# Performance work log

Measured on AMD Instinct MI355X. Metric: run time of the kernel, lower is better.

Reference implementation:

```python
import jax, jax.numpy as jnp
import numpy as np

B, N, T = 32, 256, 256
W, H, EMB = 32, 128, 64          # window_size, tgcn_hidden_dim, gsl_embed_dim
K, ALPHA, NC, E = 3, 1.0, 16, 8192  # gsl_avg_steps, gsl_alpha, num_classes, static edges
GCN_IN = W + H                    # GSL gconv in_channels
THRESH = 1e-8


def setup_inputs():
    ks = jax.random.split(jax.random.key(0), 24)
    rng = np.random.default_rng(0)
    src = rng.integers(0, N, size=E)
    tgt = (src + 1 + rng.integers(0, N - 1, size=E)) % N  # no self-loops (PyG adds them)
    edge_index = jnp.asarray(np.stack([src, tgt]), dtype=jnp.int32)

    def p(k, shape):
        return jax.random.normal(k, shape, jnp.float32) * (shape[0] ** -0.5)

    z = lambda n: jnp.zeros((n,), jnp.float32)
    return {
        "x": jax.random.normal(ks[0], (B, N, T), jnp.float32),
        "static_edge_index": edge_index,
        "static_edge_weight": jax.random.uniform(ks[1], (E,), jnp.float32),
        "Wg": p(ks[2], (GCN_IN, EMB)), "bg": z(EMB),
        "W1": p(ks[3], (EMB, EMB)), "b1": z(EMB),
        "W2": p(ks[4], (EMB, EMB)), "b2": z(EMB),
        "Wz": p(ks[5], (W, H)), "bz": z(H),
        "Wr": p(ks[6], (W, H)), "br": z(H),
        "Wh": p(ks[7], (W, H)), "bh": z(H),
        "Wlz": p(ks[8], (2 * H, H)), "blz": z(H),
        "Wlr": p(ks[9], (2 * H, H)), "blr": z(H),
        "Wlh": p(ks[10], (2 * H, H)), "blh": z(H),
        "Wc": p(ks[11], (H * N, NC)), "bc": z(NC),
    }


def _forward(x, edge_index, edge_weight, Wg, bg, W1, b1, W2, b2,
             Wz, bz, Wr, br, Wh, bh, Wlz, blz, Wlr, blr, Wlh, blh, Wc, bc):
    dt = x.dtype
    eye = jnp.eye(N, dtype=dt)

    # Static graph: dense adjacency + self loops, symmetric GCN normalization.
    A = jnp.zeros((N, N), dt).at[edge_index[0], edge_index[1]].add(edge_weight) + eye
    deg = A.sum(0)  # in-degree at targets (col sums)
    di = jnp.where(deg > 0, jax.lax.rsqrt(deg), 0.0)
    S = di[:, None] * A * di[None, :]  # S[r,c]; out[c] = sum_r S[r,c] x[r]

    # windowing: v[t,b,n,:] = x[b,n,t*W:(t+1)*W]
    v = x.reshape(B, N, T // W, W).transpose(2, 0, 1, 3)  # [nw,B,N,W]

    def gcn_norm_b(Ad):  # Ad [B,N,N], zero diagonal guaranteed
        Ah = Ad + eye
        d = Ah.sum(-2)
        q = jnp.where(d > 0, jax.lax.rsqrt(d), 0.0)
        return q[:, :, None] * Ah * q[:, None, :]

    def step(carry, vt):
        h, hist, cnt = carry  # h [B,N,H], hist [K,B,N,N]
        It = jnp.concatenate([vt, h], -1)                   # [B,N,W+H]
        df = jnp.einsum('rc,brf->bcf', S, It @ Wg) + bg     # static GCNConv
        de1 = jnp.tanh(ALPHA * (df @ W1 + b1))
        de2 = jnp.tanh(ALPHA * (df @ W2 + b2))
        M = jnp.einsum('bne,bme->bnm', de1, de2)            # de1 @ de2^T
        Et = jax.nn.relu(jnp.tanh(ALPHA * (M - M.transpose(0, 2, 1))))
        hist = jnp.concatenate([hist[1:], Et[None]], 0)     # deque(maxlen=K)
        cnt = jnp.minimum(cnt + 1, K)
        Mt = hist.sum(0) / cnt.astype(dt)
        An = gcn_norm_b(jnp.where(Mt > THRESH, Mt, jnp.zeros((), dt)))

        def conv(Wk, bk):  # dynamic GCNConv, block-diag == per-batch dense
            return jnp.einsum('brc,brf->bcf', An, vt @ Wk) + bk

        Z = jax.nn.sigmoid(jnp.concatenate([conv(Wz, bz), h], -1) @ Wlz + blz)
        R = jax.nn.sigmoid(jnp.concatenate([conv(Wr, br), h], -1) @ Wlr + blr)
        Ht = jnp.tanh(jnp.concatenate([conv(Wh, bh), h * R], -1) @ Wlh + blh)
        h = Z * h + (1.0 - Z) * Ht
        return (h, hist, cnt), None

    h0 = jnp.zeros((B, N, H), dt)
    hist0 = jnp.zeros((K, B, N, N), dt)
    (h, _, _), _ = jax.lax.scan(step, (h0, hist0, jnp.int32(0)), v)
    return h.reshape(B, N * H) @ Wc + bc  # [B, NC]


def reference(x, static_edge_index, static_edge_weight, Wg, bg, W1, b1, W2, b2,
              Wz, bz, Wr, br, Wh, bh, Wlz, blz, Wlr, blr, Wlh, blh, Wc, bc):
    return _forward(x, static_edge_index, static_edge_weight, Wg, bg, W1, b1, W2, b2,
                    Wz, bz, Wr, br, Wh, bh, Wlz, blz, Wlr, blr, Wlh, blh, Wc, bc)
```

## Files before the change

kernel.cpp:

```cpp
#include <hip/hip_runtime.h>
#include <hip/hip_bf16.h>
#include <math.h>

#define BB  32
#define NN  256
#define TT  256
#define WW  32
#define HH  128
#define EMBD 64
#define NCLS 16
#define NE  8192

__device__ __forceinline__ float bf(const __hip_bfloat16* p, int i) {
    return __bfloat162float(p[i]);
}
__device__ __forceinline__ float ld3(const void* p, int i, int m) {
    if (m == 2) return (float)((const double*)p)[i];
    if (m == 1) return ((const float*)p)[i];
    return __bfloat162float(((const __hip_bfloat16*)p)[i]);
}
__device__ __forceinline__ float r16(float x) {
    return __bfloat162float(__float2bfloat16(x));
}
__device__ __forceinline__ float tanh_s(float x) {
    x = fminf(20.0f, fmaxf(-20.0f, x));
    return tanhf(x);
}
__device__ __forceinline__ float sig_s(float x) {
    x = fminf(30.0f, fmaxf(-30.0f, x));
    return 1.0f / (1.0f + expf(-x));
}


__global__ __launch_bounds__(64) void k_sentinel(float* out, float v) {
    int i = blockIdx.x * 64 + threadIdx.x;
    if (i < BB * NCLS) out[i] = v;
}

__global__ __launch_bounds__(256) void k_probe_all(
        const void* x, const void* ew, const void* Wg, const void* W1, const void* W2,
        const void* Wz, const void* Wr, const void* Wh, const void* Wlz, const void* Wlr,
        const void* Wlh, const void* Wc, int* insB, int* insF) {
    int sec = blockIdx.x >> 2, sub = blockIdx.x & 3;
    const void* p; int nB, idx;
    switch (sec) {
        case 0:  p = x;   nB = 32768; idx = 0;  break;
        case 1:  p = ew;  nB = 8192;  idx = 2;  break;
        case 2:  p = Wg;  nB = 10240; idx = 3;  break;
        case 3:  p = W1;  nB = 4096;  idx = 5;  break;
        case 4:  p = W2;  nB = 4096;  idx = 7;  break;
        case 5:  p = Wz;  nB = 4096;  idx = 9;  break;
        case 6:  p = Wr;  nB = 4096;  idx = 11; break;
        case 7:  p = Wh;  nB = 4096;  idx = 13; break;
        case 8:  p = Wlz; nB = 32768; idx = 15; break;
        case 9:  p = Wlr; nB = 32768; idx = 17; break;
        case 10: p = Wlh; nB = 32768; idx = 19; break;
        default: p = Wc;  nB = 32768; idx = 21; break;
    }
    int nF = nB >> 2;
    const __hip_bfloat16* pb = (const __hip_bfloat16*)p;
    const float* pf = (const float*)p;
    int start = sub * 256 + threadIdx.x;
    for (int i = start; i < nB; i += 1024) {
        float v = __bfloat162float(pb[i]);
        if (!(fabsf(v) < 64.0f)) { insB[idx] = 1; break; }
    }
    for (int i = start; i < nF; i += 1024) {
        float v = pf[i];
        if (!(fabsf(v) < 1e4f)) { insF[idx] = 1; break; }
    }
}

__global__ void k_resolve(const int* insB, const int* insF, int* modes) {
    int i = threadIdx.x;
    if (i < 32 && i != 1)
        modes[i] = insB[i] ? (insF[i] ? 2 : 1) : 0;
}

__global__ __launch_bounds__(64) void k_detect_ei(const int* ei, int* modes) {
    if (threadIdx.x == 0 && blockIdx.x == 0) {
        bool allz = true;
        for (int k = 1; k < 64; k += 2) if (ei[k] != 0) allz = false;
        modes[1] = allz ? 1 : 0;
    }
}

__global__ __launch_bounds__(256) void k_cvtall(const void* Wg, const void* W1, const void* W2,
                                                const void* Wz, const void* Wr, const void* Wh,
                                                const void* Wlz, const void* Wlr, const void* Wlh,
                                                const void* Wc, const int* modes, float* dst) {
    int i = blockIdx.x * 256 + threadIdx.x;
    if (i >= 665600) return;
    float v;
    if      (i < 10240)  v = ld3(Wg,  i,          modes[3]);
    else if (i < 14336)  v = ld3(W1,  i - 10240,  modes[5]);
    else if (i < 18432)  v = ld3(W2,  i - 14336,  modes[7]);
    else if (i < 22528)  v = ld3(Wz,  i - 18432,  modes[9]);
    else if (i < 26624)  v = ld3(Wr,  i - 22528,  modes[11]);
    else if (i < 30720)  v = ld3(Wh,  i - 26624,  modes[13]);
    else if (i < 63488)  v = ld3(Wlz, i - 30720,  modes[15]);
    else if (i < 96256)  v = ld3(Wlr, i - 63488,  modes[17]);
    else if (i < 129024) v = ld3(Wlh, i - 96256,  modes[19]);
    else if (i < 653312) v = ld3(Wc,  i - 129024, modes[21]);
    else {
        int j = i - 653312, w = j / 384, rem = j - w * 384;
        int g = rem >> 7, f = rem & 127;
        const void* Wk = (g == 0) ? Wz : ((g == 1) ? Wr : Wh);
        int mk = (g == 0) ? modes[9] : ((g == 1) ? modes[11] : modes[13]);
        v = ld3(Wk, w * 128 + f, mk);
    }
    dst[i] = v;
}

__global__ __launch_bounds__(256) void k_fuse(const float* Wzf, const float* Wrf, const float* Whf,
                                              const float* Wlzf, const float* Wlrf, const float* Wlhf,
                                              const __hip_bfloat16* bz, const __hip_bfloat16* br,
                                              const __hip_bfloat16* bh,
                                              const __hip_bfloat16* blz, const __hip_bfloat16* blr,
                                              const __hip_bfloat16* blh,
                                              float* Wf, float* bfv) {
    int g = blockIdx.y;
    const float* Wcv = (g == 0) ? Wzf : ((g == 1) ? Wrf : Whf);
    const float* Wl  = (g == 0) ? Wlzf : ((g == 1) ? Wlrf : Wlhf);
    const __hip_bfloat16* bcv = (g == 0) ? bz : ((g == 1) ? br : bh);
    const __hip_bfloat16* blv = (g == 0) ? blz : ((g == 1) ? blr : blh);
    int idx = blockIdx.x * 256 + threadIdx.x;
    if (idx >= 160 * 128) return;
    int k = idx >> 7, f = idx & 127;
    float v;
    if (k < 32) {
        float acc = 0.f;
        for (int m = 0; m < 128; m++) acc += Wcv[k * 128 + m] * Wl[m * 128 + f];
        v = acc;
    } else {
        v = Wl[(k + 96) * 128 + f];
    }
    Wf[((size_t)g * 160 + k) * 128 + f] = v;
    if (idx < 128) {
        float acc = __bfloat162float(blv[idx]);
        for (int m = 0; m < 128; m++) acc += __bfloat162float(bcv[m]) * Wl[m * 128 + idx];
        bfv[g * 128 + idx] = acc;
    }
}


__global__ __launch_bounds__(256) void k_scatter(const int* ei, const void* ew, float* A,
                                                 const int* modes) {
    int e = blockIdx.x * 256 + threadIdx.x;
    if (e < NE) {
        int s, t;
        if (modes[1]) { s = ei[2 * e]; t = ei[2 * (NE + e)]; }
        else          { s = ei[e];     t = ei[NE + e]; }
        float w = r16(ld3(ew, e, modes[2]));
        if ((unsigned)s < NN && (unsigned)t < NN)
            atomicAdd(&A[s * NN + t], w);
    }
    if (blockIdx.x == 0) atomicAdd(&A[threadIdx.x * NN + threadIdx.x], 1.0f);
}

__global__ __launch_bounds__(256) void k_roundA(float* A) {
    int i = blockIdx.x * 256 + threadIdx.x;
    A[i] = r16(A[i]);
}

__global__ __launch_bounds__(256) void k_di(const float* A, float* di) {
    int wave = threadIdx.x >> 6, lane = threadIdx.x & 63;
    int c = blockIdx.x * 4 + wave;
    float s = 0.f;
    for (int r = lane; r < NN; r += 64) s += A[r * NN + c];
    for (int o = 32; o > 0; o >>= 1) s += __shfl_down(s, o, 64);
    if (lane == 0) {
        float deg = r16(s);
        di[c] = (deg > 0.f) ? r16(1.0f / sqrtf(deg)) : 0.0f;
    }
}

__global__ __launch_bounds__(256) void k_St(const float* A, const float* di, float* St) {
    int idx = blockIdx.x * 256 + threadIdx.x;
    int c = idx >> 8, r = idx & 255;
    St[idx] = r16(r16(di[r] * A[r * NN + c]) * di[c]);
}


__global__ __launch_bounds__(256) void k1_itwg4(const void* x, const float* h,
                                                const float* Wgf, float* Y,
                                                int t, const int* modes) {
    __shared__ float vt[4][32];
    __shared__ float hr[4][128];
    int b = blockIdx.y, n0 = blockIdx.x * 4;
    int tid = threadIdx.x;
    int nd = tid >> 6, f = tid & 63;
    if (f < WW) vt[nd][f] = ld3(x, (b * NN + n0 + nd) * TT + t * WW + f, modes[0]);
    size_t hb = (size_t)(b * NN + n0 + nd) * HH;
    hr[nd][f] = h[hb + f];
    hr[nd][f + 64] = h[hb + f + 64];
    __syncthreads();
    float acc = 0.f;
    for (int k = 0; k < WW; k++)  acc += vt[nd][k] * Wgf[k * EMBD + f];
    for (int k = 0; k < HH; k++)  acc += hr[nd][k] * Wgf[(WW + k) * EMBD + f];
    if (t == 0 && modes[0] == 0 && modes[3] == 0) acc = r16(acc);
    Y[(size_t)(b * NN + n0 + nd) * EMBD + f] = acc;
}

__global__ __launch_bounds__(256) void k23g(const float* St, const float* Y,
                                            const __hip_bfloat16* bg,
                                            const float* W1f, const float* W2f,
                                            const __hip_bfloat16* b1, const __hip_bfloat16* b2,
                                            float* de1, float* de2, float* qsum,
                                            int t, const int* modes) {
    __shared__ float As[32][36];
    __shared__ float Bs[32][68];
    __shared__ float dfT[64][36];
    int b = blockIdx.y, c0 = blockIdx.x * 32;
    int tid = threadIdx.x;
    if (blockIdx.x == 0) qsum[b * NN + tid] = 0.f;
    int tm = tid >> 4, tn = tid & 15;
    int am = tid & 31, ak0 = (tid >> 5) * 4;
    int bk = tid >> 3, bn0 = (tid & 7) * 8;
    const float* Yb = Y + (size_t)b * (NN * EMBD);
    float acc[2][4] = {};
    for (int kb = 0; kb < 256; kb += 32) {
        float4 a0 = *(const float4*)(St + (size_t)(c0 + am) * 256 + kb + ak0);
        float av4[4] = {a0.x, a0.y, a0.z, a0.w};
        int rot = (tid >> 5) & 3;
#pragma unroll
        for (int jj = 0; jj < 4; jj++) { int j = (jj + rot) & 3; As[ak0 + j][am] = av4[j]; }
        const float* bp = Yb + (size_t)(kb + bk) * 64 + bn0;
        *(float4*)&Bs[bk][bn0]     = *(const float4*)bp;
        *(float4*)&Bs[bk][bn0 + 4] = *(const float4*)(bp + 4);
        __syncthreads();
#pragma unroll
        for (int kk = 0; kk < 32; kk++) {
            float2 av = *(const float2*)&As[kk][tm * 2];
            float4 bv = *(const float4*)&Bs[kk][tn * 4];
            float aa[2] = {av.x, av.y};
            float bb[4] = {bv.x, bv.y, bv.z, bv.w};
#pragma unroll
            for (int i = 0; i < 2; i++)
#pragma unroll
                for (int j = 0; j < 4; j++) acc[i][j] += aa[i] * bb[j];
        }
        __syncthreads();
    }
    bool rnd = (t == 0 && modes[0] == 0 && modes[3] == 0);
#pragma unroll
    for (int i = 0; i < 2; i++)
#pragma unroll
        for (int j = 0; j < 4; j++) {
            int f = tn * 4 + j;
            float v = (rnd ? r16(acc[i][j]) : acc[i][j]) + bf(bg, f);
            dfT[f][tm * 2 + i] = v;
        }
    __syncthreads();
    float a1acc[2][4] = {};
    for (int kb2 = 0; kb2 < 64; kb2 += 32) {
        const float* bp = W1f + (size_t)(kb2 + bk) * 64 + bn0;
        *(float4*)&Bs[bk][bn0]     = *(const float4*)bp;
        *(float4*)&Bs[bk][bn0 + 4] = *(const float4*)(bp + 4);
        __syncthreads();
#pragma unroll
        for (int kk = 0; kk < 32; kk++) {
            float2 av = *(const float2*)&dfT[kb2 + kk][tm * 2];
            float4 bv = *(const float4*)&Bs[kk][tn * 4];
            float aa[2] = {av.x, av.y};
            float bb[4] = {bv.x, bv.y, bv.z, bv.w};
#pragma unroll
            for (int i = 0; i < 2; i++)
#pragma unroll
                for (int j = 0; j < 4; j++) a1acc[i][j] += aa[i] * bb[j];
        }
        __syncthreads();
    }
#pragma unroll
    for (int i = 0; i < 2; i++) {
        int row = b * NN + c0 + tm * 2 + i;
        float4 o;
        o.x = tanh_s(a1acc[i][0] + bf(b1, tn * 4 + 0));
        o.y = tanh_s(a1acc[i][1] + bf(b1, tn * 4 + 1));
        o.z = tanh_s(a1acc[i][2] + bf(b1, tn * 4 + 2));
        o.w = tanh_s(a1acc[i][3] + bf(b1, tn * 4 + 3));
        *(float4*)&de1[(size_t)row * 64 + tn * 4] = o;
    }
    float a2acc[2][4] = {};
    for (int kb2 = 0; kb2 < 64; kb2 += 32) {
        const float* bp = W2f + (size_t)(kb2 + bk) * 64 + bn0;
        *(float4*)&Bs[bk][bn0]     = *(const float4*)bp;
        *(float4*)&Bs[bk][bn0 + 4] = *(const float4*)(bp + 4);
        __syncthreads();
#pragma unroll
        for (int kk = 0; kk < 32; kk++) {
            float2 av = *(const float2*)&dfT[kb2 + kk][tm * 2];
            float4 bv = *(const float4*)&Bs[kk][tn * 4];
            float aa[2] = {av.x, av.y};
            float bb[4] = {bv.x, bv.y, bv.z, bv.w};
#pragma unroll
            for (int i = 0; i < 2; i++)
#pragma unroll
                for (int j = 0; j < 4; j++) a2acc[i][j] += aa[i] * bb[j];
        }
        __syncthreads();
    }
#pragma unroll
    for (int i = 0; i < 2; i++) {
        int row = b * NN + c0 + tm * 2 + i;
        float4 o;
        o.x = tanh_s(a2acc[i][0] + bf(b2, tn * 4 + 0));
        o.y = tanh_s(a2acc[i][1] + bf(b2, tn * 4 + 1));
        o.z = tanh_s(a2acc[i][2] + bf(b2, tn * 4 + 2));
        o.w = tanh_s(a2acc[i][3] + bf(b2, tn * 4 + 3));
        *(float4*)&de2[(size_t)row * 64 + tn * 4] = o;
    }
}

__global__ __launch_bounds__(256) void k45(const float* de1, const float* de2,
                                           float* hist, float* AhT, float* qsum,
                                           int slabW, int slabR, float inv_cnt) {
    __shared__ float As[32][68];
    __shared__ float Bs[32][68];
    __shared__ float m2b[64][65];
    __shared__ float qpart[64];
    int b = blockIdx.z, r0 = blockIdx.x * 64, c0 = blockIdx.y * 64;
    int tid = threadIdx.x;
    if (tid < 64) qpart[tid] = 0.f;
    int tn = tid & 15, tm = tid >> 4;
    int am = tid >> 2, ak0 = (tid & 3) * 8;
    int rot = (tid & 3) * 2;
    const float* d1 = de1 + (size_t)b * (NN * EMBD);
    const float* d2 = de2 + (size_t)b * (NN * EMBD);
    float acc2[4][4] = {};
    for (int kb = 0; kb < 64; kb += 32) {
        const float* ap = d1 + (size_t)(c0 + am) * 64 + kb + ak0;
        float4 a0 = *(const float4*)ap;
        float4 a1 = *(const float4*)(ap + 4);
        float av8[8] = {a0.x, a0.y, a0.z, a0.w, a1.x, a1.y, a1.z, a1.w};
#pragma unroll
        for (int jj = 0; jj < 8; jj++) { int j = (jj + rot) & 7; As[ak0 + j][am] = av8[j]; }
        const float* bp = d2 + (size_t)(r0 + am) * 64 + kb + ak0;
        float4 b0 = *(const float4*)bp;
        float4 b1v = *(const float4*)(bp + 4);
        float bv8[8] = {b0.x, b0.y, b0.z, b0.w, b1v.x, b1v.y, b1v.z, b1v.w};
#pragma unroll
        for (int jj = 0; jj < 8; jj++) { int j = (jj + rot) & 7; Bs[ak0 + j][am] = bv8[j]; }
        __syncthreads();
#pragma unroll
        for (int kk = 0; kk < 32; kk++) {
            float4 av = *(const float4*)&As[kk][tm * 4];
            float4 bv = *(const float4*)&Bs[kk][tn * 4];
            float aa[4] = {av.x, av.y, av.z, av.w};
            float bb[4] = {bv.x, bv.y, bv.z, bv.w};
#pragma unroll
            for (int i = 0; i < 4; i++)
#pragma unroll
                for (int j = 0; j < 4; j++) acc2[i][j] += aa[i] * bb[j];
        }
        __syncthreads();
    }
#pragma unroll
    for (int i = 0; i < 4; i++)
#pragma unroll
        for (int j = 0; j < 4; j++) m2b[tm * 4 + i][tn * 4 + j] = acc2[i][j];
    float acc1[4][4] = {};
    for (int kb = 0; kb < 64; kb += 32) {
        const float* ap = d1 + (size_t)(r0 + am) * 64 + kb + ak0;
        float4 a0 = *(const float4*)ap;
        float4 a1 = *(const float4*)(ap + 4);
        float av8[8] = {a0.x, a0.y, a0.z, a0.w, a1.x, a1.y, a1.z, a1.w};
#pragma unroll
        for (int jj = 0; jj < 8; jj++) { int j = (jj + rot) & 7; As[ak0 + j][am] = av8[j]; }
        const float* bp = d2 + (size_t)(c0 + am) * 64 + kb + ak0;
        float4 b0 = *(const float4*)bp;
        float4 b1v = *(const float4*)(bp + 4);
        float bv8[8] = {b0.x, b0.y, b0.z, b0.w, b1v.x, b1v.y, b1v.z, b1v.w};
#pragma unroll
        for (int jj = 0; jj < 8; jj++) { int j = (jj + rot) & 7; Bs[ak0 + j][am] = bv8[j]; }
        __syncthreads();
#pragma unroll
        for (int kk = 0; kk < 32; kk++) {
            float4 av = *(const float4*)&As[kk][tm * 4];
            float4 bv = *(const float4*)&Bs[kk][tn * 4];
            float aa[4] = {av.x, av.y, av.z, av.w};
            float bb[4] = {bv.x, bv.y, bv.z, bv.w};
#pragma unroll
            for (int i = 0; i < 4; i++)
#pragma unroll
                for (int j = 0; j < 4; j++) acc1[i][j] += aa[i] * bb[j];
        }
        __syncthreads();
    }
    size_t NB = (size_t)BB * NN * NN;
    float* hsW = hist + (size_t)slabW * NB;
    const float* hsR = hist + (size_t)slabR * NB;
    float ad[4][4];
#pragma unroll
    for (int i = 0; i < 4; i++) {
        int r = r0 + tm * 4 + i;
        size_t o = ((size_t)(b * NN + r)) * NN + c0 + tn * 4;
        float4 e2v = *(const float4*)&hsW[o];
        float4 e1v = *(const float4*)&hsR[o];
        float e2a[4] = {e2v.x, e2v.y, e2v.z, e2v.w};
        float e1a[4] = {e1v.x, e1v.y, e1v.z, e1v.w};
        float4 ew4;
        float eo[4];
#pragma unroll
        for (int j = 0; j < 4; j++) {
            int c = c0 + tn * 4 + j;
            float e = tanh_s(acc1[i][j] - m2b[tn * 4 + j][tm * 4 + i]);
            e = e > 0.f ? e : 0.f;
            eo[j] = e;
            float mt = (e + e1a[j] + e2a[j]) * inv_cnt;
            float adv = (mt > 1e-8f) ? mt : 0.f;
            if (r == c) adv += 1.f;
            ad[i][j] = adv;
        }
        ew4.x = eo[0]; ew4.y = eo[1]; ew4.z = eo[2]; ew4.w = eo[3];
        *(float4*)&hsW[o] = ew4;
    }
#pragma unroll
    for (int j = 0; j < 4; j++) {
        float cs = ad[0][j] + ad[1][j] + ad[2][j] + ad[3][j];
        atomicAdd(&qpart[tn * 4 + j], cs);
    }
    __syncthreads();
#pragma unroll
    for (int i = 0; i < 4; i++)
#pragma unroll
        for (int j = 0; j < 4; j++) m2b[tn * 4 + j][tm * 4 + i] = ad[i][j];
    __syncthreads();
#pragma unroll
    for (int kk = 0; kk < 4; kk++) {
        int e = tid + kk * 256;
        int cl = e >> 4, q4 = e & 15;
        float4 o;
        o.x = m2b[cl][q4 * 4 + 0]; o.y = m2b[cl][q4 * 4 + 1];
        o.z = m2b[cl][q4 * 4 + 2]; o.w = m2b[cl][q4 * 4 + 3];
        *(float4*)&AhT[((size_t)(b * NN + c0 + cl)) * NN + r0 + q4 * 4] = o;
    }
    if (tid < 64) atomicAdd(&qsum[b * NN + c0 + tid], qpart[tid]);
}

__global__ __launch_bounds__(256) void k8a(const float* AhT, const void* x, const float* qsum,
                                           float* G, int t, const int* modes) {
    __shared__ float As[32][36];
    __shared__ float Bs[32][36];
    int b = blockIdx.y, c0 = blockIdx.x * 32;
    int tid = threadIdx.x;
    int tm = tid >> 3, tn = tid & 7;
    int am = tid & 31, ak0 = (tid >> 5) * 8;
    int rB = tid >> 3, w0 = (tid & 7) * 4;
    int m0 = modes[0];
    const float* Ab = AhT + (size_t)b * (NN * NN);
    float acc[4] = {0, 0, 0, 0};
    for (int kb = 0; kb < 256; kb += 32) {
        const float* ap = Ab + (size_t)(c0 + am) * 256 + kb + ak0;
        float4 a0 = *(const float4*)ap;
        float4 a1 = *(const float4*)(ap + 4);
        float av8[8] = {a0.x, a0.y, a0.z, a0.w, a1.x, a1.y, a1.z, a1.w};
#pragma unroll
        for (int j = 0; j < 8; j++) As[ak0 + j][am] = av8[j];
        int r = kb + rB;
        float qr = 1.0f / sqrtf(fmaxf(qsum[b * NN + r], 1e-12f));
        int xbase = (b * NN + r) * TT + t * WW + w0;
        float pv[4];
#pragma unroll
        for (int i = 0; i < 4; i++) pv[i] = qr * ld3(x, xbase + i, m0);
        int rot = rB & 3;
#pragma unroll
        for (int i = 0; i < 4; i++) {
            int j = (i + rot) & 3;
            Bs[rB][w0 + j] = pv[j];
        }
        __syncthreads();
#pragma unroll
        for (int kk = 0; kk < 32; kk++) {
            float a = As[kk][tm];
            float4 bv = *(const float4*)&Bs[kk][tn * 4];
            acc[0] += a * bv.x; acc[1] += a * bv.y;
            acc[2] += a * bv.z; acc[3] += a * bv.w;
        }
        __syncthreads();
    }
    int c = c0 + tm;
    float qc = 1.0f / sqrtf(fmaxf(qsum[b * NN + c], 1e-12f));
    float4 o = make_float4(qc * acc[0], qc * acc[1], qc * acc[2], qc * acc[3]);
    *(float4*)&G[((size_t)(b * NN + c)) * 32 + tn * 4] = o;
}

__global__ __launch_bounds__(256) void k9f(const float* G, float* h,
                                           const float* Wf, const float* bfv) {
    __shared__ float Gs[16][36];
    __shared__ float hs[16][132];
    __shared__ float h2[16][132];
    __shared__ float Bs[32][132];
    int r0 = blockIdx.x * 16;
    int tid = threadIdx.x;
    if (tid < 128) {
        int r = tid >> 3, k4 = (tid & 7) * 4;
        *(float4*)&Gs[r][k4] = *(const float4*)&G[(size_t)(r0 + r) * 32 + k4];
    }
    {
        int e0 = tid * 2;
#pragma unroll
        for (int u = 0; u < 2; u++) {
            int e = e0 + u;
            int r = e >> 5, c4 = (e & 31) * 4;
            *(float4*)&hs[r][c4] = *(const float4*)&h[(size_t)(r0 + r) * 128 + c4];
        }
    }
    __syncthreads();
    int tm = tid >> 4, tn = tid & 15;
    float zv[2][4], rv[2][4];
    for (int g = 0; g < 2; g++) {
        float acc[2][4] = {};
        const float* Wgp = Wf + (size_t)g * (160 * 128);
        for (int kb = 0; kb < 160; kb += 32) {
#pragma unroll
            for (int j4 = 0; j4 < 4; j4++) {
                int e = tid + j4 * 256;
                int kk = e >> 5, c4 = (e & 31) * 4;
                *(float4*)&Bs[kk][c4] = *(const float4*)&Wgp[(size_t)(kb + kk) * 128 + c4];
            }
            __syncthreads();
            if (kb == 0) {
#pragma unroll
                for (int kk = 0; kk < 32; kk++) {
                    float a = Gs[tm][kk];
                    float4 b0 = *(const float4*)&Bs[kk][tn * 4];
                    float4 b1 = *(const float4*)&Bs[kk][64 + tn * 4];
                    acc[0][0] += a * b0.x; acc[0][1] += a * b0.y;
                    acc[0][2] += a * b0.z; acc[0][3] += a * b0.w;
                    acc[1][0] += a * b1.x; acc[1][1] += a * b1.y;
                    acc[1][2] += a * b1.z; acc[1][3] += a * b1.w;
                }
            } else {
#pragma unroll
                for (int kk = 0; kk < 32; kk++) {
                    float a = hs[tm][kb - 32 + kk];
                    float4 b0 = *(const float4*)&Bs[kk][tn * 4];
                    float4 b1 = *(const float4*)&Bs[kk][64 + tn * 4];
                    acc[0][0] += a * b0.x; acc[0][1] += a * b0.y;
                    acc[0][2] += a * b0.z; acc[0][3] += a * b0.w;
                    acc[1][0] += a * b1.x; acc[1][1] += a * b1.y;
                    acc[1][2] += a * b1.z; acc[1][3] += a * b1.w;
                }
            }
            __syncthreads();
        }
#pragma unroll
        for (int ci = 0; ci < 2; ci++)
#pragma unroll
            for (int j = 0; j < 4; j++) {
                int col = ci * 64 + tn * 4 + j;
                float v = sig_s(acc[ci][j] + bfv[g * 128 + col]);
                if (g == 0) zv[ci][j] = v; else rv[ci][j] = v;
            }
    }
#pragma unroll
    for (int ci = 0; ci < 2; ci++)
#pragma unroll
        for (int j = 0; j < 4; j++) {
            int col = ci * 64 + tn * 4 + j;
            h2[tm][col] = hs[tm][col] * rv[ci][j];
        }
    __syncthreads();
    float acc[2][4] = {};
    const float* Wgp = Wf + (size_t)2 * (160 * 128);
    for (int kb = 0; kb < 160; kb += 32) {
#pragma unroll
        for (int j4 = 0; j4 < 4; j4++) {
            int e = tid + j4 * 256;
            int kk = e >> 5, c4 = (e & 31) * 4;
            *(float4*)&Bs[kk][c4] = *(const float4*)&Wgp[(size_t)(kb + kk) * 128 + c4];
        }
        __syncthreads();
        if (kb == 0) {
#pragma unroll
            for (int kk = 0; kk < 32; kk++) {
                float a = Gs[tm][kk];
                float4 b0 = *(const float4*)&Bs[kk][tn * 4];
                float4 b1 = *(const float4*)&Bs[kk][64 + tn * 4];
                acc[0][0] += a * b0.x; acc[0][1] += a * b0.y;
                acc[0][2] += a * b0.z; acc[0][3] += a * b0.w;
                acc[1][0] += a * b1.x; acc[1][1] += a * b1.y;
                acc[1][2] += a * b1.z; acc[1][3] += a * b1.w;
            }
        } else {
#pragma unroll
            for (int kk = 0; kk < 32; kk++) {
                float a = h2[tm][kb - 32 + kk];
                float4 b0 = *(const float4*)&Bs[kk][tn * 4];
                float4 b1 = *(const float4*)&Bs[kk][64 + tn * 4];
                acc[0][0] += a * b0.x; acc[0][1] += a * b0.y;
                acc[0][2] += a * b0.z; acc[0][3] += a * b0.w;
                acc[1][0] += a * b1.x; acc[1][1] += a * b1.y;
                acc[1][2] += a * b1.z; acc[1][3] += a * b1.w;
            }
        }
        __syncthreads();
    }
#pragma unroll
    for (int ci = 0; ci < 2; ci++)
#pragma unroll
        for (int j = 0; j < 4; j++) {
            int col = ci * 64 + tn * 4 + j;
            float ht = tanh_s(acc[ci][j] + bfv[256 + col]);
            float hold = hs[tm][col];
            float z = zv[ci][j];
            h[(size_t)(r0 + tm) * 128 + col] = z * hold + (1.0f - z) * ht;
        }
}

__global__ __launch_bounds__(256) void k10a(const float* h, const float* Wcf, float* partial) {
    __shared__ float red[16][17];
    int chunk = blockIdx.x, b = blockIdx.y;
    int c = threadIdx.x & 15, isub = threadIdx.x >> 4;
    const float* hb = h + (size_t)b * (NN * HH);
    int i0 = chunk * 2048;
    float acc = 0.f;
    for (int s = 0; s < 128; s++) {
        int i = i0 + isub + 16 * s;
        acc += hb[i] * Wcf[(size_t)i * NCLS + c];
    }
    red[isub][c] = acc;
    __syncthreads();
    for (int st = 8; st > 0; st >>= 1) {
        if (isub < st) red[isub][c] += red[isub + st][c];
        __syncthreads();
    }
    if (isub == 0) partial[((size_t)(b * NCLS + c)) * 16 + chunk] = red[0][c];
}

__global__ __launch_bounds__(512) void k10b(const float* partial, const __hip_bfloat16* bcb,
                                            float* out) {
    int tid = threadIdx.x;
    if (tid < BB * NCLS) {
        int c = tid & 15;
        float s = 0.f;
        for (int k = 0; k < 16; k++) s += partial[(size_t)tid * 16 + k];
        out[tid] = s + bf(bcb, c);
    }
}


extern "C" void kernel_launch(void* const* d_in, const int* in_sizes, int n_in,
                              void* d_out, int out_size, void* d_ws, size_t ws_size,
                              hipStream_t stream) {
    float* out = (float*)d_out;

    static const int exp_sizes[23] = {2097152, 16384, 8192, 10240, 64, 4096, 64, 4096, 64,
                                      4096, 128, 4096, 128, 4096, 128, 32768, 128, 32768, 128,
                                      32768, 128, 524288, 16};
    if (n_in != 23) { k_sentinel<<<8, 64, 0, stream>>>(out, 4444.0f); return; }
    for (int i = 0; i < 23; i++) {
        if (in_sizes[i] != exp_sizes[i]) {
            k_sentinel<<<8, 64, 0, stream>>>(out, (float)(4000 + i));
            return;
        }
    }

    const void* x   = d_in[0];
    const int*  ei  = (const int*)d_in[1];
    const void* ew  = d_in[2];
    const void* Wg  = d_in[3];
    const __hip_bfloat16* bg  = (const __hip_bfloat16*)d_in[4];
    const void* W1  = d_in[5];
    const __hip_bfloat16* b1  = (const __hip_bfloat16*)d_in[6];
    const void* W2  = d_in[7];
    const __hip_bfloat16* b2  = (const __hip_bfloat16*)d_in[8];
    const void* Wz  = d_in[9];
    const __hip_bfloat16* bz  = (const __hip_bfloat16*)d_in[10];
    const void* Wr  = d_in[11];
    const __hip_bfloat16* br  = (const __hip_bfloat16*)d_in[12];
    const void* Wh  = d_in[13];
    const __hip_bfloat16* bh  = (const __hip_bfloat16*)d_in[14];
    const void* Wlz = d_in[15];
    const __hip_bfloat16* blz = (const __hip_bfloat16*)d_in[16];
    const void* Wlr = d_in[17];
    const __hip_bfloat16* blr = (const __hip_bfloat16*)d_in[18];
    const void* Wlh = d_in[19];
    const __hip_bfloat16* blh = (const __hip_bfloat16*)d_in[20];
    const void* Wc  = d_in[21];
    const __hip_bfloat16* bcb = (const __hip_bfloat16*)d_in[22];

    float* ws = (float*)d_ws;
    const size_t off_A    = 0;
    const size_t off_hist = off_A + 65536;
    const size_t off_h    = off_hist + 2u * 2097152;
    const size_t off_flag = off_h + 1048576;
    const size_t off_mode = off_flag + 16;
    const size_t off_insB = off_mode + 32;
    const size_t off_insF = off_insB + 32;
    const size_t zero_end = off_insF + 32;
    const size_t off_St   = zero_end;
    const size_t off_di   = off_St + 65536;
    const size_t off_q    = off_di + 256;
    const size_t off_AhT  = off_q + 8192;
    const size_t off_Yp   = off_AhT + 2097152;
    const size_t off_C    = off_Yp + 3145728;
    const size_t off_wts  = off_C + 3145728;
    const size_t need_bytes = (off_wts + 665600u) * sizeof(float);

    if (ws_size < need_bytes) {
        k_sentinel<<<8, 64, 0, stream>>>(out, (float)ws_size);
        return;
    }

    float* A    = ws + off_A;
    float* hist = ws + off_hist;
    float* h    = ws + off_h;
    int*   modes= (int*)(ws + off_mode);
    int*   insB = (int*)(ws + off_insB);
    int*   insF = (int*)(ws + off_insF);
    float* St   = ws + off_St;
    float* di   = ws + off_di;
    float* qsum = ws + off_q;
    float* AhT  = ws + off_AhT;
    float* wts  = ws + off_wts;
    float* Y    = ws + off_Yp;
    float* de1  = ws + off_Yp + 1048576;
    float* de2  = ws + off_Yp + 1572864;
    float* G    = ws + off_Yp + 2097152;
    float* Wf   = ws + off_C;
    float* bfv  = ws + off_C + 61440;
    float* partial = qsum;

    float* Wgf  = wts;
    float* W1f  = wts + 10240;
    float* W2f  = wts + 14336;
    float* Wzf  = wts + 18432;
    float* Wrf  = wts + 22528;
    float* Whf  = wts + 26624;
    float* Wlzf = wts + 30720;
    float* Wlrf = wts + 63488;
    float* Wlhf = wts + 96256;
    float* Wcf  = wts + 129024;

    hipMemsetAsync(ws, 0, zero_end * sizeof(float), stream);

    k_probe_all<<<48, 256, 0, stream>>>(x, ew, Wg, W1, W2, Wz, Wr, Wh, Wlz, Wlr, Wlh, Wc,
                                        insB, insF);
    k_resolve<<<1, 32, 0, stream>>>(insB, insF, modes);
    k_detect_ei<<<1, 64, 0, stream>>>(ei, modes);
    k_cvtall<<<2600, 256, 0, stream>>>(Wg, W1, W2, Wz, Wr, Wh, Wlz, Wlr, Wlh, Wc, modes, wts);
    k_fuse<<<dim3(80, 3), 256, 0, stream>>>(Wzf, Wrf, Whf, Wlzf, Wlrf, Wlhf,
                                            bz, br, bh, blz, blr, blh, Wf, bfv);

    k_scatter<<<NE / 256, 256, 0, stream>>>(ei, ew, A, modes);
    k_roundA<<<NN * NN / 256, 256, 0, stream>>>(A);
    k_di<<<NN / 4, 256, 0, stream>>>(A, di);
    k_St<<<NN * NN / 256, 256, 0, stream>>>(A, di, St);

    for (int t = 0; t < 8; t++) {
        k1_itwg4<<<dim3(NN / 4, BB), 256, 0, stream>>>(x, h, Wgf, Y, t, modes);
        k23g<<<dim3(8, BB), 256, 0, stream>>>(St, Y, bg, W1f, W2f, b1, b2,
                                              de1, de2, qsum, t, modes);
        float inv_cnt = 1.0f / (float)((t + 1 < 3) ? (t + 1) : 3);
        k45<<<dim3(4, 4, BB), 256, 0, stream>>>(de1, de2, hist, AhT, qsum,
                                                t & 1, (t + 1) & 1, inv_cnt);
        k8a<<<dim3(NN / 32, BB), 256, 0, stream>>>(AhT, x, qsum, G, t, modes);
        k9f<<<512, 256, 0, stream>>>(G, h, Wf, bfv);
    }

    k10a<<<dim3(16, BB), 256, 0, stream>>>(h, Wcf, partial);
    k10b<<<1, 512, 0, stream>>>(partial, bcb, out);
}
```

Before: 955.1 us.

## Fuse graph aggregation, GRU update and next-step input projection into one kernel

Merges the normalized-adjacency aggregation kernel (k8a) and the GRU gate kernel (k9f) into a single kernel, k89f, in which each block computes its 16 rows of G in shared memory instead of writing them to global memory. The same kernel then computes the next timestep's Wg projection Y from the freshly updated h, so k1_itwg4 only runs at t=0. This removes two launches per step and the G round trip. In exchange, each block recomputes the scaled x window for all 256 rows of its batch and reuses a shared pool, which adds redundant global reads and more shared-memory pressure.

```diff
diff --git a/kernel.cpp b/kernel.cpp
--- a/kernel.cpp
+++ b/kernel.cpp
@@ -438,75 +438,68 @@
     if (tid < 64) atomicAdd(&qsum[b * NN + c0 + tid], qpart[tid]);
 }
 
-__global__ __launch_bounds__(256) void k8a(const float* AhT, const void* x, const float* qsum,
-                                           float* G, int t, const int* modes) {
-    __shared__ float As[32][36];
-    __shared__ float Bs[32][36];
-    int b = blockIdx.y, c0 = blockIdx.x * 32;
+__global__ __launch_bounds__(256) void k89f(const float* AhT, const void* x, const float* qsum,
+                                            float* h, const float* Wf, const float* bfv,
+                                            const float* Wgf, float* Y, int t, const int* modes) {
+    __shared__ float qrow[256];
+    __shared__ float Gs[16 * 36];
+    __shared__ float hs[16 * 132];
+    __shared__ float pool[6336];
+    int bidx = blockIdx.x;
+    int b = bidx >> 4;
+    int r0 = (bidx & 15) * 16;
     int tid = threadIdx.x;
-    int tm = tid >> 3, tn = tid & 7;
-    int am = tid & 31, ak0 = (tid >> 5) * 8;
-    int rB = tid >> 3, w0 = (tid & 7) * 4;
     int m0 = modes[0];
-    const float* Ab = AhT + (size_t)b * (NN * NN);
-    float acc[4] = {0, 0, 0, 0};
-    for (int kb = 0; kb < 256; kb += 32) {
-        const float* ap = Ab + (size_t)(c0 + am) * 256 + kb + ak0;
-        float4 a0 = *(const float4*)ap;
-        float4 a1 = *(const float4*)(ap + 4);
-        float av8[8] = {a0.x, a0.y, a0.z, a0.w, a1.x, a1.y, a1.z, a1.w};
-#pragma unroll
-        for (int j = 0; j < 8; j++) As[ak0 + j][am] = av8[j];
-        int r = kb + rB;
-        float qr = 1.0f / sqrtf(fmaxf(qsum[b * NN + r], 1e-12f));
-        int xbase = (b * NN + r) * TT + t * WW + w0;
-        float pv[4];
-#pragma unroll
-        for (int i = 0; i < 4; i++) pv[i] = qr * ld3(x, xbase + i, m0);
-        int rot = rB & 3;
-#pragma unroll
-        for (int i = 0; i < 4; i++) {
-            int j = (i + rot) & 3;
-            Bs[rB][w0 + j] = pv[j];
-        }
-        __syncthreads();
-#pragma unroll
-        for (int kk = 0; kk < 32; kk++) {
-            float a = As[kk][tm];
-            float4 bv = *(const float4*)&Bs[kk][tn * 4];
-            acc[0] += a * bv.x; acc[1] += a * bv.y;
-            acc[2] += a * bv.z; acc[3] += a * bv.w;
-        }
-        __syncthreads();
-    }
-    int c = c0 + tm;
-    float qc = 1.0f / sqrtf(fmaxf(qsum[b * NN + c], 1e-12f));
-    float4 o = make_float4(qc * acc[0], qc * acc[1], qc * acc[2], qc * acc[3]);
-    *(float4*)&G[((size_t)(b * NN + c)) * 32 + tn * 4] = o;
-}
-
-__global__ __launch_bounds__(256) void k9f(const float* G, float* h,
-                                           const float* Wf, const float* bfv) {
-    __shared__ float Gs[16][36];
-    __shared__ float hs[16][132];
-    __shared__ float h2[16][132];
-    __shared__ float Bs[32][132];
-    int r0 = blockIdx.x * 16;
-    int tid = threadIdx.x;
-    if (tid < 128) {
-        int r = tid >> 3, k4 = (tid & 7) * 4;
-        *(float4*)&Gs[r][k4] = *(const float4*)&G[(size_t)(r0 + r) * 32 + k4];
-    }
+    float* vtq = pool;
+    float* Ah  = pool + 4096;
+
     {
         int e0 = tid * 2;
 #pragma unroll
         for (int u = 0; u < 2; u++) {
             int e = e0 + u;
             int r = e >> 5, c4 = (e & 31) * 4;
-            *(float4*)&hs[r][c4] = *(const float4*)&h[(size_t)(r0 + r) * 128 + c4];
-        }
-    }
+            *(float4*)&hs[r * 132 + c4] = *(const float4*)&h[(size_t)(bidx * 16 + r) * HH + c4];
+        }
+    }
+    qrow[tid] = 1.0f / sqrtf(fmaxf(qsum[b * NN + tid], 1e-12f));
     __syncthreads();
+
+    float gacc[2] = {0.f, 0.f};
+    int gi = tid & 15, gw = (tid >> 4) * 2;
+    for (int half = 0; half < 2; half++) {
+        int wv = tid & 31, rb = tid >> 5;
+#pragma unroll
+        for (int k = 0; k < 16; k++) {
+            int rl = rb + 8 * k;
+            int rg = half * 128 + rl;
+            vtq[rl * 32 + wv] = qrow[rg] * ld3(x, (b * NN + rg) * TT + t * WW + wv, m0);
+        }
+        {
+            int i = tid >> 4, c8 = (tid & 15) * 8;
+            const float* ap = AhT + ((size_t)(b * NN + r0 + i)) * NN + half * 128 + c8;
+            float4 a0 = *(const float4*)ap;
+            float4 a1 = *(const float4*)(ap + 4);
+            *(float4*)&Ah[i * 132 + c8]     = a0;
+            *(float4*)&Ah[i * 132 + c8 + 4] = a1;
+        }
+        __syncthreads();
+        for (int r = 0; r < 128; r++) {
+            float a = Ah[gi * 132 + r];
+            float2 v = *(const float2*)&vtq[r * 32 + gw];
+            gacc[0] += a * v.x;
+            gacc[1] += a * v.y;
+        }
+        __syncthreads();
+    }
+    {
+        float qc = qrow[r0 + gi];
+        Gs[gi * 36 + gw]     = qc * gacc[0];
+        Gs[gi * 36 + gw + 1] = qc * gacc[1];
+    }
+
+    float* h2 = pool;
+    float* Bs = pool + 2112;
     int tm = tid >> 4, tn = tid & 15;
     float zv[2][4], rv[2][4];
     for (int g = 0; g < 2; g++) {
@@ -517,15 +510,15 @@
             for (int j4 = 0; j4 < 4; j4++) {
                 int e = tid + j4 * 256;
                 int kk = e >> 5, c4 = (e & 31) * 4;
-                *(float4*)&Bs[kk][c4] = *(const float4*)&Wgp[(size_t)(kb + kk) * 128 + c4];
+                *(float4*)&Bs[kk * 132 + c4] = *(const float4*)&Wgp[(size_t)(kb + kk) * 128 + c4];
             }
             __syncthreads();
             if (kb == 0) {
 #pragma unroll
                 for (int kk = 0; kk < 32; kk++) {
-                    float a = Gs[tm][kk];
-                    float4 b0 = *(const float4*)&Bs[kk][tn * 4];
-                    float4 b1 = *(const float4*)&Bs[kk][64 + tn * 4];
+                    float a = Gs[tm * 36 + kk];
+                    float4 b0 = *(const float4*)&Bs[kk * 132 + tn * 4];
+                    float4 b1 = *(const float4*)&Bs[kk * 132 + 64 + tn * 4];
                     acc[0][0] += a * b0.x; acc[0][1] += a * b0.y;
                     acc[0][2] += a * b0.z; acc[0][3] += a * b0.w;
                     acc[1][0] += a * b1.x; acc[1][1] += a * b1.y;
@@ -534,9 +527,9 @@
             } else {
 #pragma unroll
                 for (int kk = 0; kk < 32; kk++) {
-                    float a = hs[tm][kb - 32 + kk];
-                    float4 b0 = *(const float4*)&Bs[kk][tn * 4];
-                    float4 b1 = *(const float4*)&Bs[kk][64 + tn * 4];
+                    float a = hs[tm * 132 + kb - 32 + kk];
+                    float4 b0 = *(const float4*)&Bs[kk * 132 + tn * 4];
+                    float4 b1 = *(const float4*)&Bs[kk * 132 + 64 + tn * 4];
                     acc[0][0] += a * b0.x; acc[0][1] += a * b0.y;
                     acc[0][2] += a * b0.z; acc[0][3] += a * b0.w;
                     acc[1][0] += a * b1.x; acc[1][1] += a * b1.y;
@@ -559,43 +552,45 @@
 #pragma unroll
         for (int j = 0; j < 4; j++) {
             int col = ci * 64 + tn * 4 + j;
-            h2[tm][col] = hs[tm][col] * rv[ci][j];
+            h2[tm * 132 + col] = hs[tm * 132 + col] * rv[ci][j];
         }
     __syncthreads();
     float acc[2][4] = {};
-    const float* Wgp = Wf + (size_t)2 * (160 * 128);
-    for (int kb = 0; kb < 160; kb += 32) {
-#pragma unroll
-        for (int j4 = 0; j4 < 4; j4++) {
-            int e = tid + j4 * 256;
-            int kk = e >> 5, c4 = (e & 31) * 4;
-            *(float4*)&Bs[kk][c4] = *(const float4*)&Wgp[(size_t)(kb + kk) * 128 + c4];
-        }
-        __syncthreads();
-        if (kb == 0) {
-#pragma unroll
-            for (int kk = 0; kk < 32; kk++) {
-                float a = Gs[tm][kk];
-                float4 b0 = *(const float4*)&Bs[kk][tn * 4];
-                float4 b1 = *(const float4*)&Bs[kk][64 + tn * 4];
-                acc[0][0] += a * b0.x; acc[0][1] += a * b0.y;
-                acc[0][2] += a * b0.z; acc[0][3] += a * b0.w;
-                acc[1][0] += a * b1.x; acc[1][1] += a * b1.y;
-                acc[1][2] += a * b1.z; acc[1][3] += a * b1.w;
+    {
+        const float* Wgp = Wf + (size_t)2 * (160 * 128);
+        for (int kb = 0; kb < 160; kb += 32) {
+#pragma unroll
+            for (int j4 = 0; j4 < 4; j4++) {
+                int e = tid + j4 * 256;
+                int kk = e >> 5, c4 = (e & 31) * 4;
+                *(float4*)&Bs[kk * 132 + c4] = *(const float4*)&Wgp[(size_t)(kb + kk) * 128 + c4];
             }
-        } else {
-#pragma unroll
-            for (int kk = 0; kk < 32; kk++) {
-                float a = h2[tm][kb - 32 + kk];
-                float4 b0 = *(const float4*)&Bs[kk][tn * 4];
-                float4 b1 = *(const float4*)&Bs[kk][64 + tn * 4];
-                acc[0][0] += a * b0.x; acc[0][1] += a * b0.y;
-                acc[0][2] += a * b0.z; acc[0][3] += a * b0.w;
-                acc[1][0] += a * b1.x; acc[1][1] += a * b1.y;
-                acc[1][2] += a * b1.z; acc[1][3] += a * b1.w;
+            __syncthreads();
+            if (kb == 0) {
+#pragma unroll
+                for (int kk = 0; kk < 32; kk++) {
+                    float a = Gs[tm * 36 + kk];
+                    float4 b0 = *(const float4*)&Bs[kk * 132 + tn * 4];
+                    float4 b1 = *(const float4*)&Bs[kk * 132 + 64 + tn * 4];
+                    acc[0][0] += a * b0.x; acc[0][1] += a * b0.y;
+                    acc[0][2] += a * b0.z; acc[0][3] += a * b0.w;
+                    acc[1][0] += a * b1.x; acc[1][1] += a * b1.y;
+                    acc[1][2] += a * b1.z; acc[1][3] += a * b1.w;
+                }
+            } else {
+#pragma unroll
+                for (int kk = 0; kk < 32; kk++) {
+                    float a = h2[tm * 132 + kb - 32 + kk];
+                    float4 b0 = *(const float4*)&Bs[kk * 132 + tn * 4];
+                    float4 b1 = *(const float4*)&Bs[kk * 132 + 64 + tn * 4];
+                    acc[0][0] += a * b0.x; acc[0][1] += a * b0.y;
+                    acc[0][2] += a * b0.z; acc[0][3] += a * b0.w;
+                    acc[1][0] += a * b1.x; acc[1][1] += a * b1.y;
+                    acc[1][2] += a * b1.z; acc[1][3] += a * b1.w;
+                }
             }
-        }
-        __syncthreads();
+            __syncthreads();
+        }
     }
 #pragma unroll
     for (int ci = 0; ci < 2; ci++)
@@ -603,10 +598,47 @@
         for (int j = 0; j < 4; j++) {
             int col = ci * 64 + tn * 4 + j;
             float ht = tanh_s(acc[ci][j] + bfv[256 + col]);
-            float hold = hs[tm][col];
+            float hold = hs[tm * 132 + col];
             float z = zv[ci][j];
-            h[(size_t)(r0 + tm) * 128 + col] = z * hold + (1.0f - z) * ht;
-        }
+            float hn = z * hold + (1.0f - z) * ht;
+            h[(size_t)(bidx * 16 + tm) * HH + col] = hn;
+            hs[tm * 132 + col] = hn;
+        }
+
+    if (t < 7) {
+        float* vt2 = pool;
+        float* Ws  = pool + 2112;
+        {
+            int e0 = tid * 2;
+#pragma unroll
+            for (int u = 0; u < 2; u++) {
+                int e = e0 + u;
+                int r = e >> 5, w = e & 31;
+                vt2[r * 33 + w] = ld3(x, (b * NN + r0 + r) * TT + (t + 1) * WW + w, m0);
+            }
+        }
+        float yacc[4] = {0.f, 0.f, 0.f, 0.f};
+        int yi = tid >> 4, yf = (tid & 15) * 4;
+        for (int kb = 0; kb < 160; kb += 32) {
+            {
+                int kk = tid >> 3, f0 = (tid & 7) * 8;
+                const float* wp = Wgf + (size_t)(kb + kk) * 64 + f0;
+                *(float4*)&Ws[kk * 68 + f0]     = *(const float4*)wp;
+                *(float4*)&Ws[kk * 68 + f0 + 4] = *(const float4*)(wp + 4);
+            }
+            __syncthreads();
+#pragma unroll
+            for (int k2 = 0; k2 < 32; k2++) {
+                float a = (kb == 0) ? vt2[yi * 33 + k2] : hs[yi * 132 + kb - 32 + k2];
+                float4 wv = *(const float4*)&Ws[k2 * 68 + yf];
+                yacc[0] += a * wv.x; yacc[1] += a * wv.y;
+                yacc[2] += a * wv.z; yacc[3] += a * wv.w;
+            }
+            __syncthreads();
+        }
+        float4 o = make_float4(yacc[0], yacc[1], yacc[2], yacc[3]);
+        *(float4*)&Y[(size_t)(bidx * 16 + yi) * 64 + yf] = o;
+    }
 }
 
 __global__ __launch_bounds__(256) void k10a(const float* h, const float* Wcf, float* partial) {
@@ -718,7 +750,6 @@
     float* Y    = ws + off_Yp;
     float* de1  = ws + off_Yp + 1048576;
     float* de2  = ws + off_Yp + 1572864;
-    float* G    = ws + off_Yp + 2097152;
     float* Wf   = ws + off_C;
     float* bfv  = ws + off_C + 61440;
     float* partial = qsum;
@@ -750,14 +781,14 @@
     k_St<<<NN * NN / 256, 256, 0, stream>>>(A, di, St);
 
     for (int t = 0; t < 8; t++) {
-        k1_itwg4<<<dim3(NN / 4, BB), 256, 0, stream>>>(x, h, Wgf, Y, t, modes);
+        if (t == 0)
+            k1_itwg4<<<dim3(NN / 4, BB), 256, 0, stream>>>(x, h, Wgf, Y, 0, modes);
         k23g<<<dim3(8, BB), 256, 0, stream>>>(St, Y, bg, W1f, W2f, b1, b2,
                                               de1, de2, qsum, t, modes);
         float inv_cnt = 1.0f / (float)((t + 1 < 3) ? (t + 1) : 3);
         k45<<<dim3(4, 4, BB), 256, 0, stream>>>(de1, de2, hist, AhT, qsum,
                                                 t & 1, (t + 1) & 1, inv_cnt);
-        k8a<<<dim3(NN / 32, BB), 256, 0, stream>>>(AhT, x, qsum, G, t, modes);
-        k9f<<<512, 256, 0, stream>>>(G, h, Wf, bfv);
+        k89f<<<512, 256, 0, stream>>>(AhT, x, qsum, h, Wf, bfv, Wgf, Y, t, modes);
     }
 
     k10a<<<dim3(16, BB), 256, 0, stream>>>(h, Wcf, partial);
```

Result: slower. 1.028 ms (+7.6%).

## Split GRU gate kernel into parallel Z/R kernel and candidate-state kernel

Applied to the files above, without the earlier changes.

The fused per-step GRU kernel, which computed the Z, R and candidate GEMMs serially in one block of 16 rows, is replaced by two kernels. The first computes Z and R in parallel across a grid dimension, 32 rows per block with 4x4 register tiles, and writes Z and h*R to workspace. The second computes the candidate state and the final h update. This raises per-thread arithmetic intensity and exposes more parallelism, at the cost of an extra launch per step and extra global traffic for Z and hR. Z reuses the de1 buffer region.

```diff
diff --git a/kernel.cpp b/kernel.cpp
--- a/kernel.cpp
+++ b/kernel.cpp
@@ -485,128 +485,139 @@
     *(float4*)&G[((size_t)(b * NN + c)) * 32 + tn * 4] = o;
 }
 
-__global__ __launch_bounds__(256) void k9f(const float* G, float* h,
-                                           const float* Wf, const float* bfv) {
-    __shared__ float Gs[16][36];
-    __shared__ float hs[16][132];
-    __shared__ float h2[16][132];
-    __shared__ float Bs[32][132];
-    int r0 = blockIdx.x * 16;
+__global__ __launch_bounds__(256) void kZR(const float* G, const float* h,
+                                           const float* Wf, const float* bfv,
+                                           float* Z, float* hR) {
+    __shared__ float As[160 * 33];
+    __shared__ float Bs[32 * 128];
+    int r0 = blockIdx.x * 32;
+    int g  = blockIdx.y;
     int tid = threadIdx.x;
-    if (tid < 128) {
-        int r = tid >> 3, k4 = (tid & 7) * 4;
-        *(float4*)&Gs[r][k4] = *(const float4*)&G[(size_t)(r0 + r) * 32 + k4];
-    }
     {
-        int e0 = tid * 2;
-#pragma unroll
-        for (int u = 0; u < 2; u++) {
-            int e = e0 + u;
-            int r = e >> 5, c4 = (e & 31) * 4;
-            *(float4*)&hs[r][c4] = *(const float4*)&h[(size_t)(r0 + r) * 128 + c4];
-        }
-    }
-    __syncthreads();
-    int tm = tid >> 4, tn = tid & 15;
-    float zv[2][4], rv[2][4];
-    for (int g = 0; g < 2; g++) {
-        float acc[2][4] = {};
-        const float* Wgp = Wf + (size_t)g * (160 * 128);
-        for (int kb = 0; kb < 160; kb += 32) {
-#pragma unroll
-            for (int j4 = 0; j4 < 4; j4++) {
-                int e = tid + j4 * 256;
-                int kk = e >> 5, c4 = (e & 31) * 4;
-                *(float4*)&Bs[kk][c4] = *(const float4*)&Wgp[(size_t)(kb + kk) * 128 + c4];
-            }
-            __syncthreads();
-            if (kb == 0) {
-#pragma unroll
-                for (int kk = 0; kk < 32; kk++) {
-                    float a = Gs[tm][kk];
-                    float4 b0 = *(const float4*)&Bs[kk][tn * 4];
-                    float4 b1 = *(const float4*)&Bs[kk][64 + tn * 4];
-                    acc[0][0] += a * b0.x; acc[0][1] += a * b0.y;
-                    acc[0][2] += a * b0.z; acc[0][3] += a * b0.w;
-                    acc[1][0] += a * b1.x; acc[1][1] += a * b1.y;
-                    acc[1][2] += a * b1.z; acc[1][3] += a * b1.w;
-                }
-            } else {
-#pragma unroll
-                for (int kk = 0; kk < 32; kk++) {
-                    float a = hs[tm][kb - 32 + kk];
-                    float4 b0 = *(const float4*)&Bs[kk][tn * 4];
-                    float4 b1 = *(const float4*)&Bs[kk][64 + tn * 4];
-                    acc[0][0] += a * b0.x; acc[0][1] += a * b0.y;
-                    acc[0][2] += a * b0.z; acc[0][3] += a * b0.w;
-                    acc[1][0] += a * b1.x; acc[1][1] += a * b1.y;
-                    acc[1][2] += a * b1.z; acc[1][3] += a * b1.w;
-                }
-            }
-            __syncthreads();
-        }
-#pragma unroll
-        for (int ci = 0; ci < 2; ci++)
-#pragma unroll
-            for (int j = 0; j < 4; j++) {
-                int col = ci * 64 + tn * 4 + j;
-                float v = sig_s(acc[ci][j] + bfv[g * 128 + col]);
-                if (g == 0) zv[ci][j] = v; else rv[ci][j] = v;
-            }
-    }
-#pragma unroll
-    for (int ci = 0; ci < 2; ci++)
-#pragma unroll
-        for (int j = 0; j < 4; j++) {
-            int col = ci * 64 + tn * 4 + j;
-            h2[tm][col] = hs[tm][col] * rv[ci][j];
-        }
-    __syncthreads();
-    float acc[2][4] = {};
+        int r = tid >> 3, c4 = (tid & 7) * 4;
+        float4 gv = *(const float4*)&G[(size_t)(r0 + r) * 32 + c4];
+        As[(c4 + 0) * 33 + r] = gv.x;
+        As[(c4 + 1) * 33 + r] = gv.y;
+        As[(c4 + 2) * 33 + r] = gv.z;
+        As[(c4 + 3) * 33 + r] = gv.w;
+    }
+#pragma unroll
+    for (int u = 0; u < 4; u++) {
+        int e = tid + u * 256;
+        int r = e >> 5, c4 = (e & 31) * 4;
+        float4 hv = *(const float4*)&h[(size_t)(r0 + r) * 128 + c4];
+        As[(32 + c4 + 0) * 33 + r] = hv.x;
+        As[(32 + c4 + 1) * 33 + r] = hv.y;
+        As[(32 + c4 + 2) * 33 + r] = hv.z;
+        As[(32 + c4 + 3) * 33 + r] = hv.w;
+    }
+    const float* Wgp = Wf + (size_t)g * (160 * 128);
+    int rg = tid >> 5, cg = tid & 31;
+    float acc[4][4] = {};
+    for (int kb = 0; kb < 160; kb += 32) {
+#pragma unroll
+        for (int u = 0; u < 4; u++) {
+            int e = tid + u * 256;
+            int kk = e >> 5, c4 = (e & 31) * 4;
+            *(float4*)&Bs[kk * 128 + c4] = *(const float4*)&Wgp[(size_t)(kb + kk) * 128 + c4];
+        }
+        __syncthreads();
+#pragma unroll 4
+        for (int kk = 0; kk < 32; kk++) {
+            const float* ap = &As[(kb + kk) * 33 + rg * 4];
+            float a0 = ap[0], a1 = ap[1], a2 = ap[2], a3 = ap[3];
+            float4 bv = *(const float4*)&Bs[kk * 128 + cg * 4];
+            acc[0][0] += a0 * bv.x; acc[0][1] += a0 * bv.y; acc[0][2] += a0 * bv.z; acc[0][3] += a0 * bv.w;
+            acc[1][0] += a1 * bv.x; acc[1][1] += a1 * bv.y; acc[1][2] += a1 * bv.z; acc[1][3] += a1 * bv.w;
+            acc[2][0] += a2 * bv.x; acc[2][1] += a2 * bv.y; acc[2][2] += a2 * bv.z; acc[2][3] += a2 * bv.w;
+            acc[3][0] += a3 * bv.x; acc[3][1] += a3 * bv.y; acc[3][2] += a3 * bv.z; acc[3][3] += a3 * bv.w;
+        }
+        __syncthreads();
+    }
+    float bb[4];
+#pragma unroll
+    for (int j = 0; j < 4; j++) bb[j] = bfv[g * 128 + cg * 4 + j];
+#pragma unroll
+    for (int i = 0; i < 4; i++) {
+        int row = r0 + rg * 4 + i;
+        float4 o;
+        o.x = sig_s(acc[i][0] + bb[0]);
+        o.y = sig_s(acc[i][1] + bb[1]);
+        o.z = sig_s(acc[i][2] + bb[2]);
+        o.w = sig_s(acc[i][3] + bb[3]);
+        if (g == 0) {
+            *(float4*)&Z[(size_t)row * 128 + cg * 4] = o;
+        } else {
+            float4 hv = *(const float4*)&h[(size_t)row * 128 + cg * 4];
+            o.x *= hv.x; o.y *= hv.y; o.z *= hv.z; o.w *= hv.w;
+            *(float4*)&hR[(size_t)row * 128 + cg * 4] = o;
+        }
+    }
+}
+
+__global__ __launch_bounds__(256) void kHt(const float* G, float* h, const float* hR,
+                                           const float* Z, const float* Wf, const float* bfv) {
+    __shared__ float As[160 * 33];
+    __shared__ float Bs[32 * 128];
+    int r0 = blockIdx.x * 32;
+    int tid = threadIdx.x;
+    {
+        int r = tid >> 3, c4 = (tid & 7) * 4;
+        float4 gv = *(const float4*)&G[(size_t)(r0 + r) * 32 + c4];
+        As[(c4 + 0) * 33 + r] = gv.x;
+        As[(c4 + 1) * 33 + r] = gv.y;
+        As[(c4 + 2) * 33 + r] = gv.z;
+        As[(c4 + 3) * 33 + r] = gv.w;
+    }
+#pragma unroll
+    for (int u = 0; u < 4; u++) {
+        int e = tid + u * 256;
+        int r = e >> 5, c4 = (e & 31) * 4;
+        float4 hv = *(const float4*)&hR[(size_t)(r0 + r) * 128 + c4];
+        As[(32 + c4 + 0) * 33 + r] = hv.x;
+        As[(32 + c4 + 1) * 33 + r] = hv.y;
+        As[(32 + c4 + 2) * 33 + r] = hv.z;
+        As[(32 + c4 + 3) * 33 + r] = hv.w;
+    }
     const float* Wgp = Wf + (size_t)2 * (160 * 128);
+    int rg = tid >> 5, cg = tid & 31;
+    float acc[4][4] = {};
     for (int kb = 0; kb < 160; kb += 32) {
 #pragma unroll
-        for (int j4 = 0; j4 < 4; j4++) {
-            int e = tid + j4 * 256;
+        for (int u = 0; u < 4; u++) {
+            int e = tid + u * 256;
             int kk = e >> 5, c4 = (e & 31) * 4;
-            *(float4*)&Bs[kk][c4] = *(const float4*)&Wgp[(size_t)(kb + kk) * 128 + c4];
-        }
-        __syncthreads();
-        if (kb == 0) {
-#pragma unroll
-            for (int kk = 0; kk < 32; kk++) {
-                float a = Gs[tm][kk];
-                float4 b0 = *(const float4*)&Bs[kk][tn * 4];
-                float4 b1 = *(const float4*)&Bs[kk][64 + tn * 4];
-                acc[0][0] += a * b0.x; acc[0][1] += a * b0.y;
-                acc[0][2] += a * b0.z; acc[0][3] += a * b0.w;
-                acc[1][0] += a * b1.x; acc[1][1] += a * b1.y;
-                acc[1][2] += a * b1.z; acc[1][3] += a * b1.w;
-            }
-        } else {
-#pragma unroll
-            for (int kk = 0; kk < 32; kk++) {
-                float a = h2[tm][kb - 32 + kk];
-                float4 b0 = *(const float4*)&Bs[kk][tn * 4];
-                float4 b1 = *(const float4*)&Bs[kk][64 + tn * 4];
-                acc[0][0] += a * b0.x; acc[0][1] += a * b0.y;
-                acc[0][2] += a * b0.z; acc[0][3] += a * b0.w;
-                acc[1][0] += a * b1.x; acc[1][1] += a * b1.y;
-                acc[1][2] += a * b1.z; acc[1][3] += a * b1.w;
-            }
-        }
-        __syncthreads();
-    }
-#pragma unroll
-    for (int ci = 0; ci < 2; ci++)
-#pragma unroll
-        for (int j = 0; j < 4; j++) {
-            int col = ci * 64 + tn * 4 + j;
-            float ht = tanh_s(acc[ci][j] + bfv[256 + col]);
-            float hold = hs[tm][col];
-            float z = zv[ci][j];
-            h[(size_t)(r0 + tm) * 128 + col] = z * hold + (1.0f - z) * ht;
-        }
+            *(float4*)&Bs[kk * 128 + c4] = *(const float4*)&Wgp[(size_t)(kb + kk) * 128 + c4];
+        }
+        __syncthreads();
+#pragma unroll 4
+        for (int kk = 0; kk < 32; kk++) {
+            const float* ap = &As[(kb + kk) * 33 + rg * 4];
+            float a0 = ap[0], a1 = ap[1], a2 = ap[2], a3 = ap[3];
+            float4 bv = *(const float4*)&Bs[kk * 128 + cg * 4];
+            acc[0][0] += a0 * bv.x; acc[0][1] += a0 * bv.y; acc[0][2] += a0 * bv.z; acc[0][3] += a0 * bv.w;
+            acc[1][0] += a1 * bv.x; acc[1][1] += a1 * bv.y; acc[1][2] += a1 * bv.z; acc[1][3] += a1 * bv.w;
+            acc[2][0] += a2 * bv.x; acc[2][1] += a2 * bv.y; acc[2][2] += a2 * bv.z; acc[2][3] += a2 * bv.w;
+            acc[3][0] += a3 * bv.x; acc[3][1] += a3 * bv.y; acc[3][2] += a3 * bv.z; acc[3][3] += a3 * bv.w;
+        }
+        __syncthreads();
+    }
+    float bb[4];
+#pragma unroll
+    for (int j = 0; j < 4; j++) bb[j] = bfv[256 + cg * 4 + j];
+#pragma unroll
+    for (int i = 0; i < 4; i++) {
+        int row = r0 + rg * 4 + i;
+        size_t o = (size_t)row * 128 + cg * 4;
+        float4 zv = *(const float4*)&Z[o];
+        float4 hv = *(const float4*)&h[o];
+        float4 r;
+        r.x = zv.x * hv.x + (1.0f - zv.x) * tanh_s(acc[i][0] + bb[0]);
+        r.y = zv.y * hv.y + (1.0f - zv.y) * tanh_s(acc[i][1] + bb[1]);
+        r.z = zv.z * hv.z + (1.0f - zv.z) * tanh_s(acc[i][2] + bb[2]);
+        r.w = zv.w * hv.w + (1.0f - zv.w) * tanh_s(acc[i][3] + bb[3]);
+        *(float4*)&h[o] = r;
+    }
 }
 
 __global__ __launch_bounds__(256) void k10a(const float* h, const float* Wcf, float* partial) {
@@ -697,7 +708,8 @@
     const size_t off_Yp   = off_AhT + 2097152;
     const size_t off_C    = off_Yp + 3145728;
     const size_t off_wts  = off_C + 3145728;
-    const size_t need_bytes = (off_wts + 665600u) * sizeof(float);
+    const size_t off_hR   = off_wts + 665600;
+    const size_t need_bytes = (off_hR + 1048576u) * sizeof(float);
 
     if (ws_size < need_bytes) {
         k_sentinel<<<8, 64, 0, stream>>>(out, (float)ws_size);
@@ -718,7 +730,9 @@
     float* Y    = ws + off_Yp;
     float* de1  = ws + off_Yp + 1048576;
     float* de2  = ws + off_Yp + 1572864;
+    float* Z    = ws + off_Yp + 1048576;
     float* G    = ws + off_Yp + 2097152;
+    float* hR   = ws + off_hR;
     float* Wf   = ws + off_C;
     float* bfv  = ws + off_C + 61440;
     float* partial = qsum;
@@ -757,7 +771,8 @@
         k45<<<dim3(4, 4, BB), 256, 0, stream>>>(de1, de2, hist, AhT, qsum,
                                                 t & 1, (t + 1) & 1, inv_cnt);
         k8a<<<dim3(NN / 32, BB), 256, 0, stream>>>(AhT, x, qsum, G, t, modes);
-        k9f<<<512, 256, 0, stream>>>(G, h, Wf, bfv);
+        kZR<<<dim3(NN * BB / 32, 2), 256, 0, stream>>>(G, h, Wf, bfv, Z, hR);
+        kHt<<<NN * BB / 32, 256, 0, stream>>>(G, h, hR, Z, Wf, bfv);
     }
 
     k10a<<<dim3(16, BB), 256, 0, stream>>>(h, Wcf, partial);
```

Measured after the change: 948.9 us. No clear change (-0.7%).
